# Optimization experiments

Measured on AMD Instinct MI355X. Metric: run time of the kernel, lower is better.

The kernel has to match this reference:

```python
import jax, jax.numpy as jnp
import numpy as np

N_NODES = 50000
N_EDGES = 800000
IN_DIM = 128
HID = 8
HEADS = 8
OUT_DIM = 64
NEG_SLOPE = 0.2


def setup_inputs() -> dict:
    key = jax.random.key(0)
    ks = jax.random.split(key, 8)
    x = jax.random.normal(ks[0], (N_NODES, IN_DIM), dtype=jnp.float32)
    edge_index = jax.random.randint(ks[1], (2, N_EDGES), 0, N_NODES, dtype=jnp.int64)
    W1 = jax.random.normal(ks[2], (IN_DIM, HEADS * HID), dtype=jnp.float32) / np.sqrt(IN_DIM)
    a_src1 = jax.random.normal(ks[3], (HEADS, HID), dtype=jnp.float32)
    a_dst1 = jax.random.normal(ks[4], (HEADS, HID), dtype=jnp.float32)
    b1 = jnp.zeros((HEADS * HID,), dtype=jnp.float32)
    W2 = jax.random.normal(ks[5], (HEADS * HID, OUT_DIM), dtype=jnp.float32) / np.sqrt(HEADS * HID)
    a_src2 = jax.random.normal(ks[6], (1, OUT_DIM), dtype=jnp.float32)
    a_dst2 = jax.random.normal(ks[7], (1, OUT_DIM), dtype=jnp.float32)
    b2 = jnp.zeros((OUT_DIM,), dtype=jnp.float32)
    return {"x": x, "edge_index": edge_index, "W1": W1, "a_src1": a_src1,
            "a_dst1": a_dst1, "b1": b1, "W2": W2, "a_src2": a_src2,
            "a_dst2": a_dst2, "b2": b2}


def gat_conv(x, src, dst, W, a_src, a_dst, b, heads, ch):
    # PyG GATConv (eval mode): linear -> per-edge LeakyReLU score ->
    # segment-softmax over incoming edges -> weighted scatter-add -> +bias
    n = x.shape[0]
    h = (x @ W).reshape(n, heads, ch)               # [N,H,C]
    score_src = jnp.einsum('nhc,hc->nh', h, a_src)  # [N,H]
    score_dst = jnp.einsum('nhc,hc->nh', h, a_dst)  # [N,H]
    e = jax.nn.leaky_relu(score_src[src] + score_dst[dst], NEG_SLOPE)  # [E,H]
    m = jax.ops.segment_max(e, dst, num_segments=n)
    m = jnp.where(jnp.isfinite(m), m, 0.0)
    p = jnp.exp(e - m[dst])
    denom = jax.ops.segment_sum(p, dst, num_segments=n)
    alpha = p / (denom[dst] + 1e-16)                # [E,H]
    out = jax.ops.segment_sum(h[src] * alpha[:, :, None], dst, num_segments=n)
    return out.reshape(n, heads * ch) + b


def reference(x, edge_index, W1, a_src1, a_dst1, b1, W2, a_src2, a_dst2, b2):
    n = x.shape[0]
    # add_self_loops=True (PyG default)
    loops = jnp.arange(n, dtype=edge_index.dtype)
    src = jnp.concatenate([edge_index[0], loops])
    dst = jnp.concatenate([edge_index[1], loops])
    h = gat_conv(x, src, dst, W1, a_src1, a_dst1, b1, HEADS, HID)
    h = jax.nn.elu(h)
    out = gat_conv(h, src, dst, W2, a_src2, a_dst2, b2, 1, OUT_DIM)
    return out
```

## Files before the change

### kernel.cpp

```cpp
#include <hip/hip_runtime.h>
#include <hip/hip_fp16.h>
#include <math.h>
#include <stdint.h>

#define N_NODES 50000
#define N_EDGES 800000
#define ET (N_EDGES + N_NODES)
#define IN_DIM 128
#define H1DIM 64
#define HEADS 8
#define HID 8
#define OUT_DIM 64
#define NEG_SLOPE 0.2f

#define SCAN_TILE 256
#define NTILES ((N_NODES + SCAN_TILE - 1) / SCAN_TILE)
#define RC 8
#define PF 6

#define LIN1_WAVES (N_NODES / 16)
#define LIN1_BLOCKS ((LIN1_WAVES + 3) / 4)
#define LIN2_WAVES (N_NODES / 16)
#define LIN2_BLOCKS ((LIN2_WAVES + 3) / 4)

#define EPT 4
#define CB ((N_EDGES + 256*EPT - 1) / (256*EPT))
#define FB CB
#define ZB ((8 * N_NODES + 255) / 256)

typedef _Float16 half8 __attribute__((ext_vector_type(8)));
typedef float f32x4 __attribute__((ext_vector_type(4)));

__device__ __forceinline__ float lrelu(float v) { return v >= 0.f ? v : NEG_SLOPE * v; }

__device__ __forceinline__ int xcc_id() {
    int v;
    asm volatile("s_getreg_b32 %0, hwreg(HW_REG_XCC_ID)" : "=s"(v));
    return v & 7;
}

__device__ __forceinline__ void fma8raw(uint4 u, float alpha, float* a) {
    float2 f0 = __half22float2(*(const __half2*)&u.x);
    float2 f1 = __half22float2(*(const __half2*)&u.y);
    float2 f2 = __half22float2(*(const __half2*)&u.z);
    float2 f3 = __half22float2(*(const __half2*)&u.w);
    a[0] += f0.x * alpha; a[1] += f0.y * alpha;
    a[2] += f1.x * alpha; a[3] += f1.y * alpha;
    a[4] += f2.x * alpha; a[5] += f2.y * alpha;
    a[6] += f3.x * alpha; a[7] += f3.y * alpha;
}

__device__ __forceinline__ void fma8h(const __half* __restrict__ base, float alpha, float* a) {
    fma8raw(*reinterpret_cast<const uint4*>(base), alpha, a);
}


__global__ __launch_bounds__(256) void prep_kernel(
    const float* __restrict__ W1, const float* __restrict__ W2,
    __half* __restrict__ w1fH, __half* __restrict__ w1fL,
    __half* __restrict__ w2fH, __half* __restrict__ w2fL,
    int* __restrict__ cnt8)
{
    int b = blockIdx.x;
    if (b < 32) {
        int idx = b * 256 + threadIdx.x;
        int f = idx >> 9, rr = idx & 511;
        int l = rr >> 3, j = rr & 7;
        int ks = f >> 2, ct = f & 3;
        int k = ks * 32 + ((l >> 4) << 3) + j;
        int c = (ct << 4) + (l & 15);
        float w = W1[k * 64 + c];
        __half hi = __float2half(w);
        w1fH[idx] = hi;
        w1fL[idx] = __float2half(w - __half2float(hi));
    } else if (b < 48) {
        int idx = (b - 32) * 256 + threadIdx.x;
        int f = idx >> 9, rr = idx & 511;
        int l = rr >> 3, j = rr & 7;
        int ks = f >> 2, ct = f & 3;
        int k = ks * 32 + ((l >> 4) << 3) + j;
        int c = (ct << 4) + (l & 15);
        float w = W2[k * 64 + c];
        __half hi = __float2half(w);
        w2fH[idx] = hi;
        w2fL[idx] = __float2half(w - __half2float(hi));
    } else {
        int i = (b - 48) * 256 + threadIdx.x;
        if (i < 8 * N_NODES) cnt8[i] = 0;
    }
}


__global__ __launch_bounds__(256) void cl1_kernel(
    const int* __restrict__ ei, int* __restrict__ cnt8, int* __restrict__ pos,
    const float* __restrict__ x,
    const __half* __restrict__ w1fH, const __half* __restrict__ w1fL,
    const float* __restrict__ a_src, const float* __restrict__ a_dst,
    __half* __restrict__ h1, float* __restrict__ ssrc, float* __restrict__ sdst)
{
    if (blockIdx.x < CB) {
        int base = blockIdx.x * (256 * EPT) + threadIdx.x;
        int c = xcc_id();
        #pragma unroll
        for (int j = 0; j < EPT; ++j) {
            int e = base + j * 256;
            if (e < N_EDGES) {
                int d = ei[N_EDGES + e];
                int r = atomicAdd(&cnt8[c * N_NODES + d], 1);
                pos[e] = r | (c << 28);
            }
        }
        return;
    }

    int wid = threadIdx.x >> 6, t = threadIdx.x & 63;
    int g = (blockIdx.x - CB) * 4 + wid;
    if (g >= LIN1_WAVES) return;
    int n0 = g * 16;
    int row = t & 15, kq = t >> 4;

    f32x4 acc[4] = {};
    const float* xp = x + (size_t)(n0 + row) * IN_DIM + kq * 8;
    #pragma unroll
    for (int ks = 0; ks < 4; ++ks) {
        float4 u0 = *reinterpret_cast<const float4*>(xp + ks * 32);
        float4 u1 = *reinterpret_cast<const float4*>(xp + ks * 32 + 4);
        float xv[8] = {u0.x, u0.y, u0.z, u0.w, u1.x, u1.y, u1.z, u1.w};
        half8 ah, al;
        #pragma unroll
        for (int j = 0; j < 8; ++j) {
            _Float16 h = (_Float16)xv[j];
            ah[j] = h;
            al[j] = (_Float16)(xv[j] - (float)h);
        }
        #pragma unroll
        for (int ct = 0; ct < 4; ++ct) {
            int f = ks * 4 + ct;
            half8 bh = *reinterpret_cast<const half8*>(w1fH + f * 512 + t * 8);
            half8 bl = *reinterpret_cast<const half8*>(w1fL + f * 512 + t * 8);
            acc[ct] = __builtin_amdgcn_mfma_f32_16x16x32_f16(ah, bh, acc[ct], 0, 0, 0);
            acc[ct] = __builtin_amdgcn_mfma_f32_16x16x32_f16(al, bh, acc[ct], 0, 0, 0);
            acc[ct] = __builtin_amdgcn_mfma_f32_16x16x32_f16(ah, bl, acc[ct], 0, 0, 0);
        }
    }

    float asv[4], adv[4];
    #pragma unroll
    for (int ct = 0; ct < 4; ++ct) {
        asv[ct] = a_src[ct * 16 + (t & 15)];
        adv[ct] = a_dst[ct * 16 + (t & 15)];
    }
    int rbase = n0 + (t >> 4) * 4;
    #pragma unroll
    for (int r = 0; r < 4; ++r) {
        int n = rbase + r;
        #pragma unroll
        for (int ct = 0; ct < 4; ++ct) {
            float v = acc[ct][r];
            h1[(size_t)n * 64 + ct * 16 + (t & 15)] = __float2half(v);
            float ps = v * asv[ct], pd = v * adv[ct];
            ps += __shfl_xor(ps, 1); ps += __shfl_xor(ps, 2); ps += __shfl_xor(ps, 4);
            pd += __shfl_xor(pd, 1); pd += __shfl_xor(pd, 2); pd += __shfl_xor(pd, 4);
            if ((t & 7) == 0) {
                int hd = ct * 2 + ((t >> 3) & 1);
                ssrc[n * 8 + hd] = ps;
                sdst[n * 8 + hd] = pd;
            }
        }
    }
}


__global__ __launch_bounds__(SCAN_TILE) void scanA_kernel(
    const int* __restrict__ cnt8, int* __restrict__ row, int* __restrict__ aux)
{
    __shared__ int sh[SCAN_TILE];
    int t = threadIdx.x, i = blockIdx.x * SCAN_TILE + t;
    int v = 0;
    if (i < N_NODES) {
        v = 1;
        #pragma unroll
        for (int c = 0; c < 8; ++c) v += cnt8[c * N_NODES + i];
    }
    sh[t] = v;
    __syncthreads();
    #pragma unroll
    for (int off = 1; off < SCAN_TILE; off <<= 1) {
        int add = (t >= off) ? sh[t - off] : 0;
        __syncthreads();
        sh[t] += add;
        __syncthreads();
    }
    if (i < N_NODES) row[i] = sh[t] - v;
    if (t == SCAN_TILE - 1) aux[blockIdx.x] = sh[t];
}

__global__ __launch_bounds__(SCAN_TILE) void scanB_kernel(int* __restrict__ aux, int* __restrict__ row) {
    __shared__ int sh[SCAN_TILE];
    int t = threadIdx.x;
    int v = (t < NTILES) ? aux[t] : 0;
    sh[t] = v;
    __syncthreads();
    #pragma unroll
    for (int off = 1; off < SCAN_TILE; off <<= 1) {
        int add = (t >= off) ? sh[t - off] : 0;
        __syncthreads();
        sh[t] += add;
        __syncthreads();
    }
    if (t < NTILES) aux[t] = sh[t] - v;
    if (t == NTILES - 1) row[N_NODES] = sh[t];
}

__global__ __launch_bounds__(SCAN_TILE) void scanC_kernel(
    const int* __restrict__ aux, int* __restrict__ row,
    const int* __restrict__ cnt8, int* __restrict__ off8, int* __restrict__ adj)
{
    int i = blockIdx.x * SCAN_TILE + threadIdx.x;
    if (i >= N_NODES) return;
    int r = row[i] + aux[i >> 8];
    row[i] = r;
    int run = r;
    #pragma unroll
    for (int c = 0; c < 8; ++c) {
        off8[c * N_NODES + i] = run;
        run += cnt8[c * N_NODES + i];
    }
    adj[run] = i;
}

__global__ __launch_bounds__(256) void fill_kernel(
    const int* __restrict__ ei, const int* __restrict__ off8,
    const int* __restrict__ pos, int* __restrict__ adj)
{
    int base = blockIdx.x * (256 * EPT) + threadIdx.x;
    #pragma unroll
    for (int j = 0; j < EPT; ++j) {
        int e = base + j * 256;
        if (e < N_EDGES) {
            int s = ei[e], d = ei[N_EDGES + e];
            int pr = pos[e];
            int c = (unsigned)pr >> 28;
            int r = pr & 0x0FFFFFFF;
            adj[off8[c * N_NODES + d] + r] = s;
        }
    }
}


__global__ __launch_bounds__(256) void l1_kernel(
    const int* __restrict__ row, const int* __restrict__ adj,
    const __half* __restrict__ h1, const float* __restrict__ s1, const float* __restrict__ t1,
    const float* __restrict__ b1, __half* __restrict__ ha)
{
    int wid = threadIdx.x >> 6, t = threadIdx.x & 63;
    int half = t >> 5, tt = t & 31;
    int n = blockIdx.x * 8 + wid * 2 + half;
    int beg = row[n], end = row[n + 1];
    int slot = tt >> 3, h = tt & 7;
    float sd = t1[n * 8 + h];
    const int e0 = beg + slot;

    int   sv[RC];
    float p[RC];
    uint4 raw[PF];
    float m = -3e38f;
    #pragma unroll
    for (int it = 0; it < RC; ++it) {
        int e = e0 + it * 4;
        bool ok = e < end;
        int s = ok ? adj[e] : n;
        sv[it] = s;
        float v = ok ? lrelu(s1[s * 8 + h] + sd) : -3e38f;
        p[it] = v;
        m = fmaxf(m, v);
        if (it < PF) raw[it] = *reinterpret_cast<const uint4*>(h1 + (size_t)s * 64 + h * 8);
    }
    for (int e = e0 + RC * 4; e < end; e += 4)
        m = fmaxf(m, lrelu(s1[adj[e] * 8 + h] + sd));
    m = fmaxf(m, __shfl_xor(m, 8));
    m = fmaxf(m, __shfl_xor(m, 16));

    float den = 0.f;
    #pragma unroll
    for (int it = 0; it < RC; ++it) {
        float pe = __expf(p[it] - m);
        p[it] = pe;
        den += pe;
    }
    for (int e = e0 + RC * 4; e < end; e += 4)
        den += __expf(lrelu(s1[adj[e] * 8 + h] + sd) - m);
    den += __shfl_xor(den, 8);
    den += __shfl_xor(den, 16);
    float inv = 1.f / (den + 1e-16f);

    float a[8] = {0,0,0,0,0,0,0,0};
    #pragma unroll
    for (int it = 0; it < PF; ++it) fma8raw(raw[it], p[it] * inv, a);
    #pragma unroll
    for (int it = PF; it < RC; ++it) {
        int e = e0 + it * 4;
        if (e < end) fma8h(h1 + (size_t)sv[it] * 64 + h * 8, p[it] * inv, a);
    }
    for (int e = e0 + RC * 4; e < end; e += 4) {
        int s = adj[e];
        float alpha = __expf(lrelu(s1[s * 8 + h] + sd) - m) * inv;
        fma8h(h1 + (size_t)s * 64 + h * 8, alpha, a);
    }
    #pragma unroll
    for (int j = 0; j < 8; ++j) {
        a[j] += __shfl_xor(a[j], 8);
        a[j] += __shfl_xor(a[j], 16);
    }

    int j0 = slot * 2;
    float v0 = a[j0]     + b1[h * 8 + j0];
    float v1 = a[j0 + 1] + b1[h * 8 + j0 + 1];
    v0 = v0 > 0.f ? v0 : (__expf(v0) - 1.f);
    v1 = v1 > 0.f ? v1 : (__expf(v1) - 1.f);
    __half2 hv;
    hv.x = __float2half(v0);
    hv.y = __float2half(v1);
    *reinterpret_cast<__half2*>(ha + (size_t)n * 64 + h * 8 + j0) = hv;
}


__global__ __launch_bounds__(256) void lin2_kernel(
    const __half* __restrict__ ha,
    const __half* __restrict__ w2fH, const __half* __restrict__ w2fL,
    const float* __restrict__ as2, const float* __restrict__ ad2,
    __half* __restrict__ h2, float* __restrict__ s2, float* __restrict__ t2)
{
    int tid = threadIdx.x;
    int wid = tid >> 6, t = tid & 63;
    int g = blockIdx.x * 4 + wid;
    if (g >= LIN2_WAVES) return;
    int n0 = g * 16;
    int row = t & 15, kq = t >> 4;

    f32x4 acc[4] = {};
    const __half* xp = ha + (size_t)(n0 + row) * 64 + kq * 8;
    #pragma unroll
    for (int ks = 0; ks < 2; ++ks) {
        half8 ahv = *reinterpret_cast<const half8*>(xp + ks * 32);
        #pragma unroll
        for (int ct = 0; ct < 4; ++ct) {
            int f = ks * 4 + ct;
            half8 bh = *reinterpret_cast<const half8*>(w2fH + f * 512 + t * 8);
            half8 bl = *reinterpret_cast<const half8*>(w2fL + f * 512 + t * 8);
            acc[ct] = __builtin_amdgcn_mfma_f32_16x16x32_f16(ahv, bh, acc[ct], 0, 0, 0);
            acc[ct] = __builtin_amdgcn_mfma_f32_16x16x32_f16(ahv, bl, acc[ct], 0, 0, 0);
        }
    }

    float asv[4], adv[4];
    #pragma unroll
    for (int ct = 0; ct < 4; ++ct) {
        asv[ct] = as2[ct * 16 + (t & 15)];
        adv[ct] = ad2[ct * 16 + (t & 15)];
    }
    int rbase = n0 + (t >> 4) * 4;
    #pragma unroll
    for (int r = 0; r < 4; ++r) {
        int n = rbase + r;
        float ps = 0.f, pd = 0.f;
        #pragma unroll
        for (int ct = 0; ct < 4; ++ct) {
            float v = acc[ct][r];
            h2[(size_t)n * 64 + ct * 16 + (t & 15)] = __float2half(v);
            ps += v * asv[ct];
            pd += v * adv[ct];
        }
        ps += __shfl_xor(ps, 1); ps += __shfl_xor(ps, 2);
        ps += __shfl_xor(ps, 4); ps += __shfl_xor(ps, 8);
        pd += __shfl_xor(pd, 1); pd += __shfl_xor(pd, 2);
        pd += __shfl_xor(pd, 4); pd += __shfl_xor(pd, 8);
        if ((t & 15) == 0) { s2[n] = ps; t2[n] = pd; }
    }
}


__global__ __launch_bounds__(256) void l2_kernel(
    const int* __restrict__ row, const int* __restrict__ adj,
    const __half* __restrict__ h2, const float* __restrict__ s2, const float* __restrict__ t2,
    const float* __restrict__ b2, float* __restrict__ out)
{
    int wid = threadIdx.x >> 6, t = threadIdx.x & 63;
    int half = t >> 5, tt = t & 31;
    int n = blockIdx.x * 8 + wid * 2 + half;
    int beg = row[n], end = row[n + 1];
    int slot = tt >> 3, g = tt & 7;
    float sd = t2[n];
    const int e0 = beg + slot;

    int   sv[RC];
    float p[RC];
    uint4 raw[PF];
    float m = -3e38f;
    #pragma unroll
    for (int it = 0; it < RC; ++it) {
        int e = e0 + it * 4;
        bool ok = e < end;
        int s = ok ? adj[e] : n;
        sv[it] = s;
        float v = ok ? lrelu(s2[s] + sd) : -3e38f;
        p[it] = v;
        m = fmaxf(m, v);
        if (it < PF) raw[it] = *reinterpret_cast<const uint4*>(h2 + (size_t)s * 64 + g * 8);
    }
    for (int e = e0 + RC * 4; e < end; e += 4)
        m = fmaxf(m, lrelu(s2[adj[e]] + sd));
    m = fmaxf(m, __shfl_xor(m, 8));
    m = fmaxf(m, __shfl_xor(m, 16));

    float den = 0.f;
    #pragma unroll
    for (int it = 0; it < RC; ++it) {
        float pe = __expf(p[it] - m);
        p[it] = pe;
        den += pe;
    }
    for (int e = e0 + RC * 4; e < end; e += 4)
        den += __expf(lrelu(s2[adj[e]] + sd) - m);
    den += __shfl_xor(den, 8);
    den += __shfl_xor(den, 16);
    float inv = 1.f / (den + 1e-16f);

    float a[8] = {0,0,0,0,0,0,0,0};
    #pragma unroll
    for (int it = 0; it < PF; ++it) fma8raw(raw[it], p[it] * inv, a);
    #pragma unroll
    for (int it = PF; it < RC; ++it) {
        int e = e0 + it * 4;
        if (e < end) fma8h(h2 + (size_t)sv[it] * 64 + g * 8, p[it] * inv, a);
    }
    for (int e = e0 + RC * 4; e < end; e += 4) {
        int s = adj[e];
        float alpha = __expf(lrelu(s2[s] + sd) - m) * inv;
        fma8h(h2 + (size_t)s * 64 + g * 8, alpha, a);
    }
    #pragma unroll
    for (int j = 0; j < 8; ++j) {
        a[j] += __shfl_xor(a[j], 8);
        a[j] += __shfl_xor(a[j], 16);
    }
    if (slot == 0) {
        float4 o0 = make_float4(a[0] + b2[g * 8 + 0], a[1] + b2[g * 8 + 1],
                                a[2] + b2[g * 8 + 2], a[3] + b2[g * 8 + 3]);
        float4 o1 = make_float4(a[4] + b2[g * 8 + 4], a[5] + b2[g * 8 + 5],
                                a[6] + b2[g * 8 + 6], a[7] + b2[g * 8 + 7]);
        float4* op = (float4*)(out + (size_t)n * 64 + g * 8);
        op[0] = o0; op[1] = o1;
    }
}

extern "C" void kernel_launch(void* const* d_in, const int* in_sizes, int n_in,
                              void* d_out, int out_size, void* d_ws, size_t ws_size,
                              hipStream_t stream)
{
    const float* x   = (const float*)d_in[0];
    const int* ei    = (const int*)d_in[1];
    const float* W1  = (const float*)d_in[2];
    const float* as1 = (const float*)d_in[3];
    const float* ad1 = (const float*)d_in[4];
    const float* b1  = (const float*)d_in[5];
    const float* W2  = (const float*)d_in[6];
    const float* as2 = (const float*)d_in[7];
    const float* ad2 = (const float*)d_in[8];
    const float* b2  = (const float*)d_in[9];
    float* out = (float*)d_out;

    char* wsb = (char*)d_ws;
    __half* h1   = (__half*)wsb;
    __half* h2   = h1 + (size_t)N_NODES * 64;
    __half* ha   = h2 + (size_t)N_NODES * 64;
    __half* w1fH = ha + (size_t)N_NODES * 64;
    __half* w1fL = w1fH + 8192;
    __half* w2fH = w1fL + 8192;
    __half* w2fL = w2fH + 4096;
    float*  s1   = (float*)(w2fL + 4096);
    float*  t1   = s1 + N_NODES * 8;
    float*  s2   = t1 + N_NODES * 8;
    float*  t2   = s2 + N_NODES;
    int*    cnt8 = (int*)(t2 + N_NODES);
    int*    off8 = cnt8 + 8 * N_NODES;
    int*    rowp = off8 + 8 * N_NODES;
    int*    aux  = rowp + N_NODES + 1;
    int*    adj  = aux + NTILES;
    int*    pos  = adj + ET;

    prep_kernel<<<48 + ZB, 256, 0, stream>>>(W1, W2, w1fH, w1fL, w2fH, w2fL, cnt8);

    cl1_kernel<<<CB + LIN1_BLOCKS, 256, 0, stream>>>(ei, cnt8, pos, x, w1fH, w1fL,
                                                     as1, ad1, h1, s1, t1);

    scanA_kernel<<<NTILES, SCAN_TILE, 0, stream>>>(cnt8, rowp, aux);
    scanB_kernel<<<1, SCAN_TILE, 0, stream>>>(aux, rowp);
    scanC_kernel<<<NTILES, SCAN_TILE, 0, stream>>>(aux, rowp, cnt8, off8, adj);
    fill_kernel<<<FB, 256, 0, stream>>>(ei, off8, pos, adj);

    l1_kernel<<<N_NODES / 8, 256, 0, stream>>>(rowp, adj, h1, s1, t1, b1, ha);

    lin2_kernel<<<LIN2_BLOCKS, 256, 0, stream>>>(ha, w2fH, w2fL, as2, ad2, h2, s2, t2);

    l2_kernel<<<N_NODES / 8, 256, 0, stream>>>(rowp, adj, h2, s2, t2, b2, out);
}
```

Baseline: 218.1 us.

## Replace per-node atomic CSR build with two-pass bucketed counting sort

The CSR construction moves from per-edge global atomics on per-XCC node counters, followed by a three-kernel scan and a scatter fill, to a coarse two-level radix sort. Edges are first histogrammed into 256-node buckets in shared memory and then partitioned into a bucket buffer. Each bucket is then sorted locally in LDS, which writes row pointers and the adjacency list, self loops included. This cuts global atomic traffic and kernel count but adds an extra pass over the edge buffer, and the order of neighbours within a row becomes nondeterministic.

```diff
diff --git a/kernel.cpp b/kernel.cpp
--- a/kernel.cpp
+++ b/kernel.cpp
@@ -13,20 +13,16 @@
 #define OUT_DIM 64
 #define NEG_SLOPE 0.2f
 
+#define NB ((N_NODES + 255) / 256)
 #define SCAN_TILE 256
-#define NTILES ((N_NODES + SCAN_TILE - 1) / SCAN_TILE)
 #define RC 8
 #define PF 6
 
 #define LIN1_WAVES (N_NODES / 16)
 #define LIN1_BLOCKS ((LIN1_WAVES + 3) / 4)
-#define LIN2_WAVES (N_NODES / 16)
-#define LIN2_BLOCKS ((LIN2_WAVES + 3) / 4)
 
 #define EPT 4
-#define CB ((N_EDGES + 256*EPT - 1) / (256*EPT))
-#define FB CB
-#define ZB ((8 * N_NODES + 255) / 256)
+#define HB ((N_EDGES + 256*EPT - 1) / (256*EPT))
 
 typedef _Float16 half8 __attribute__((ext_vector_type(8)));
 typedef float f32x4 __attribute__((ext_vector_type(4)));
@@ -59,7 +55,7 @@
     const float* __restrict__ W1, const float* __restrict__ W2,
     __half* __restrict__ w1fH, __half* __restrict__ w1fL,
     __half* __restrict__ w2fH, __half* __restrict__ w2fL,
-    int* __restrict__ cnt8)
+    int* __restrict__ gb8)
 {
     int b = blockIdx.x;
     if (b < 32) {
@@ -85,36 +81,39 @@
         w2fH[idx] = hi;
         w2fL[idx] = __float2half(w - __half2float(hi));
     } else {
-        int i = (b - 48) * 256 + threadIdx.x;
-        if (i < 8 * N_NODES) cnt8[i] = 0;
+        for (int k = threadIdx.x; k < 8 * NB; k += 256) gb8[k] = 0;
     }
 }
 
 
 __global__ __launch_bounds__(256) void cl1_kernel(
-    const int* __restrict__ ei, int* __restrict__ cnt8, int* __restrict__ pos,
+    const int* __restrict__ ei, int* __restrict__ gb8,
     const float* __restrict__ x,
     const __half* __restrict__ w1fH, const __half* __restrict__ w1fL,
     const float* __restrict__ a_src, const float* __restrict__ a_dst,
     __half* __restrict__ h1, float* __restrict__ ssrc, float* __restrict__ sdst)
 {
-    if (blockIdx.x < CB) {
+    __shared__ int hist[NB];
+    if (blockIdx.x < HB) {
+        for (int k = threadIdx.x; k < NB; k += 256) hist[k] = 0;
+        __syncthreads();
         int base = blockIdx.x * (256 * EPT) + threadIdx.x;
-        int c = xcc_id();
         #pragma unroll
         for (int j = 0; j < EPT; ++j) {
             int e = base + j * 256;
-            if (e < N_EDGES) {
-                int d = ei[N_EDGES + e];
-                int r = atomicAdd(&cnt8[c * N_NODES + d], 1);
-                pos[e] = r | (c << 28);
-            }
+            if (e < N_EDGES) atomicAdd(&hist[ei[N_EDGES + e] >> 8], 1);
+        }
+        __syncthreads();
+        int c = xcc_id();
+        if (threadIdx.x < NB) {
+            int h = hist[threadIdx.x];
+            if (h) atomicAdd(&gb8[c * NB + threadIdx.x], h);
         }
         return;
     }
 
     int wid = threadIdx.x >> 6, t = threadIdx.x & 63;
-    int g = (blockIdx.x - CB) * 4 + wid;
+    int g = (blockIdx.x - HB) * 4 + wid;
     if (g >= LIN1_WAVES) return;
     int n0 = g * 16;
     int row = t & 15, kq = t >> 4;
@@ -171,18 +170,18 @@
 }
 
 
-__global__ __launch_bounds__(SCAN_TILE) void scanA_kernel(
-    const int* __restrict__ cnt8, int* __restrict__ row, int* __restrict__ aux)
+__global__ __launch_bounds__(SCAN_TILE) void bscan_kernel(
+    const int* __restrict__ gb8, int* __restrict__ ebase, int* __restrict__ cursor,
+    int* __restrict__ rowp)
 {
     __shared__ int sh[SCAN_TILE];
-    int t = threadIdx.x, i = blockIdx.x * SCAN_TILE + t;
-    int v = 0;
-    if (i < N_NODES) {
-        v = 1;
-        #pragma unroll
-        for (int c = 0; c < 8; ++c) v += cnt8[c * N_NODES + i];
-    }
-    sh[t] = v;
+    int t = threadIdx.x;
+    int cnt = 0;
+    if (t < NB) {
+        #pragma unroll
+        for (int c = 0; c < 8; ++c) cnt += gb8[c * NB + t];
+    }
+    sh[t] = cnt;
     __syncthreads();
     #pragma unroll
     for (int off = 1; off < SCAN_TILE; off <<= 1) {
@@ -191,60 +190,93 @@
         sh[t] += add;
         __syncthreads();
     }
-    if (i < N_NODES) row[i] = sh[t] - v;
-    if (t == SCAN_TILE - 1) aux[blockIdx.x] = sh[t];
-}
-
-__global__ __launch_bounds__(SCAN_TILE) void scanB_kernel(int* __restrict__ aux, int* __restrict__ row) {
-    __shared__ int sh[SCAN_TILE];
-    int t = threadIdx.x;
-    int v = (t < NTILES) ? aux[t] : 0;
-    sh[t] = v;
-    __syncthreads();
-    #pragma unroll
-    for (int off = 1; off < SCAN_TILE; off <<= 1) {
-        int add = (t >= off) ? sh[t - off] : 0;
+    if (t < NB) {
+        int e = sh[t] - cnt;
+        ebase[t] = e;
+        cursor[t] = e;
+    }
+    if (t == NB - 1) ebase[NB] = sh[t];
+    if (t == 0) rowp[N_NODES] = ET;
+}
+
+
+__global__ __launch_bounds__(256) void p1_kernel(
+    const int* __restrict__ ei, int* __restrict__ cursor, int* __restrict__ ebuf)
+{
+    __shared__ int hist[NB];
+    __shared__ int res[NB];
+    for (int k = threadIdx.x; k < NB; k += 256) hist[k] = 0;
+    __syncthreads();
+
+    int base = blockIdx.x * (256 * EPT) + threadIdx.x;
+    int ss[EPT], ds[EPT];
+    #pragma unroll
+    for (int j = 0; j < EPT; ++j) {
+        int e = base + j * 256;
+        ds[j] = -1;
+        if (e < N_EDGES) {
+            ss[j] = ei[e];
+            ds[j] = ei[N_EDGES + e];
+            atomicAdd(&hist[ds[j] >> 8], 1);
+        }
+    }
+    __syncthreads();
+    if (threadIdx.x < NB) {
+        int h = hist[threadIdx.x];
+        res[threadIdx.x] = h ? atomicAdd(&cursor[threadIdx.x], h) : 0;
+        hist[threadIdx.x] = 0;
+    }
+    __syncthreads();
+    #pragma unroll
+    for (int j = 0; j < EPT; ++j) {
+        if (ds[j] >= 0) {
+            int b = ds[j] >> 8;
+            int r = atomicAdd(&hist[b], 1);
+            ebuf[res[b] + r] = ss[j] | ((ds[j] & 255) << 16);
+        }
+    }
+}
+
+
+__global__ __launch_bounds__(256) void p2_kernel(
+    const int* __restrict__ ebase, const int* __restrict__ ebuf,
+    int* __restrict__ rowp, int* __restrict__ adj)
+{
+    __shared__ int cnt[256];
+    __shared__ int sh[256];
+    __shared__ int off[256];
+    __shared__ int cur[256];
+    int b = blockIdx.x, t = threadIdx.x;
+    int n0 = b * 256;
+    int nn = N_NODES - n0; if (nn > 256) nn = 256;
+    cnt[t] = (t < nn) ? 1 : 0;
+    __syncthreads();
+    int ebeg = ebase[b], eend = ebase[b + 1];
+    for (int e = ebeg + t; e < eend; e += 256)
+        atomicAdd(&cnt[ebuf[e] >> 16], 1);
+    __syncthreads();
+    int myc = cnt[t];
+    sh[t] = myc;
+    __syncthreads();
+    #pragma unroll
+    for (int o = 1; o < 256; o <<= 1) {
+        int add = (t >= o) ? sh[t - o] : 0;
         __syncthreads();
         sh[t] += add;
         __syncthreads();
     }
-    if (t < NTILES) aux[t] = sh[t] - v;
-    if (t == NTILES - 1) row[N_NODES] = sh[t];
-}
-
-__global__ __launch_bounds__(SCAN_TILE) void scanC_kernel(
-    const int* __restrict__ aux, int* __restrict__ row,
-    const int* __restrict__ cnt8, int* __restrict__ off8, int* __restrict__ adj)
-{
-    int i = blockIdx.x * SCAN_TILE + threadIdx.x;
-    if (i >= N_NODES) return;
-    int r = row[i] + aux[i >> 8];
-    row[i] = r;
-    int run = r;
-    #pragma unroll
-    for (int c = 0; c < 8; ++c) {
-        off8[c * N_NODES + i] = run;
-        run += cnt8[c * N_NODES + i];
-    }
-    adj[run] = i;
-}
-
-__global__ __launch_bounds__(256) void fill_kernel(
-    const int* __restrict__ ei, const int* __restrict__ off8,
-    const int* __restrict__ pos, int* __restrict__ adj)
-{
-    int base = blockIdx.x * (256 * EPT) + threadIdx.x;
-    #pragma unroll
-    for (int j = 0; j < EPT; ++j) {
-        int e = base + j * 256;
-        if (e < N_EDGES) {
-            int s = ei[e], d = ei[N_EDGES + e];
-            int pr = pos[e];
-            int c = (unsigned)pr >> 28;
-            int r = pr & 0x0FFFFFFF;
-            adj[off8[c * N_NODES + d] + r] = s;
-        }
-    }
+    int ab = ebeg + n0;
+    int myoff = ab + sh[t] - myc;
+    off[t] = myoff;
+    cur[t] = myoff;
+    if (t < nn) rowp[n0 + t] = myoff;
+    __syncthreads();
+    for (int e = ebeg + t; e < eend; e += 256) {
+        int v = ebuf[e];
+        int r = atomicAdd(&cur[v >> 16], 1);
+        adj[r] = v & 0xFFFF;
+    }
+    if (t < nn) adj[myoff + myc - 1] = n0 + t;
 }
 
 
@@ -334,7 +366,7 @@
     int tid = threadIdx.x;
     int wid = tid >> 6, t = tid & 63;
     int g = blockIdx.x * 4 + wid;
-    if (g >= LIN2_WAVES) return;
+    if (g >= LIN1_WAVES) return;
     int n0 = g * 16;
     int row = t & 15, kq = t >> 4;
 
@@ -482,26 +514,25 @@
     float*  t1   = s1 + N_NODES * 8;
     float*  s2   = t1 + N_NODES * 8;
     float*  t2   = s2 + N_NODES;
-    int*    cnt8 = (int*)(t2 + N_NODES);
-    int*    off8 = cnt8 + 8 * N_NODES;
-    int*    rowp = off8 + 8 * N_NODES;
-    int*    aux  = rowp + N_NODES + 1;
-    int*    adj  = aux + NTILES;
-    int*    pos  = adj + ET;
-
-    prep_kernel<<<48 + ZB, 256, 0, stream>>>(W1, W2, w1fH, w1fL, w2fH, w2fL, cnt8);
-
-    cl1_kernel<<<CB + LIN1_BLOCKS, 256, 0, stream>>>(ei, cnt8, pos, x, w1fH, w1fL,
+    int*    gb8  = (int*)(t2 + N_NODES);
+    int*    ebase= gb8 + 8 * NB;
+    int*    cursor = ebase + NB + 1;
+    int*    rowp = cursor + NB;
+    int*    adj  = rowp + N_NODES + 1;
+    int*    ebuf = adj + ET;
+
+    prep_kernel<<<49, 256, 0, stream>>>(W1, W2, w1fH, w1fL, w2fH, w2fL, gb8);
+
+    cl1_kernel<<<HB + LIN1_BLOCKS, 256, 0, stream>>>(ei, gb8, x, w1fH, w1fL,
                                                      as1, ad1, h1, s1, t1);
 
-    scanA_kernel<<<NTILES, SCAN_TILE, 0, stream>>>(cnt8, rowp, aux);
-    scanB_kernel<<<1, SCAN_TILE, 0, stream>>>(aux, rowp);
-    scanC_kernel<<<NTILES, SCAN_TILE, 0, stream>>>(aux, rowp, cnt8, off8, adj);
-    fill_kernel<<<FB, 256, 0, stream>>>(ei, off8, pos, adj);
+    bscan_kernel<<<1, SCAN_TILE, 0, stream>>>(gb8, ebase, cursor, rowp);
+    p1_kernel<<<HB, 256, 0, stream>>>(ei, cursor, ebuf);
+    p2_kernel<<<NB, 256, 0, stream>>>(ebase, ebuf, rowp, adj);
 
     l1_kernel<<<N_NODES / 8, 256, 0, stream>>>(rowp, adj, h1, s1, t1, b1, ha);
 
-    lin2_kernel<<<LIN2_BLOCKS, 256, 0, stream>>>(ha, w2fH, w2fL, as2, ad2, h2, s2, t2);
+    lin2_kernel<<<LIN1_BLOCKS, 256, 0, stream>>>(ha, w2fH, w2fL, as2, ad2, h2, s2, t2);
 
     l2_kernel<<<N_NODES / 8, 256, 0, stream>>>(rowp, adj, h2, s2, t2, b2, out);
 }
```

New measurement: 214.5 us. No clear change (-1.6%).
